# Performance work log

Measured on AMD Instinct MI355X. Metric: run time of the kernel, lower is better.

The kernel has to match this reference:

```python
import jax, jax.numpy as jnp
import numpy as np

D_MODEL = 1152
NUM_HEADS = 16
HEAD_DIM = D_MODEL // NUM_HEADS
B, N, M = 8, 4096, 300


def setup_inputs() -> dict:
    key = jax.random.key(0)
    ks = jax.random.split(key, 10)
    s = 0.02
    x = jax.random.normal(ks[0], (B, N, D_MODEL), dtype=jnp.float32)
    cond = jax.random.normal(ks[1], (B, M, D_MODEL), dtype=jnp.float32)
    # per-sample valid conditioning lengths in [1, M]
    mask = jax.random.randint(ks[2], (B,), 1, M + 1, dtype=jnp.int32)
    wq = jax.random.normal(ks[3], (D_MODEL, D_MODEL), dtype=jnp.float32) * s
    bq = jnp.zeros((D_MODEL,), dtype=jnp.float32)
    wkv = jax.random.normal(ks[4], (D_MODEL, 2 * D_MODEL), dtype=jnp.float32) * s
    bkv = jnp.zeros((2 * D_MODEL,), dtype=jnp.float32)
    wp = jax.random.normal(ks[5], (D_MODEL, D_MODEL), dtype=jnp.float32) * s
    bp = jnp.zeros((D_MODEL,), dtype=jnp.float32)
    return {"x": x, "cond": cond, "mask": mask, "wq": wq, "bq": bq,
            "wkv": wkv, "bkv": bkv, "wp": wp, "bp": bp}


def reference(x, cond, mask, wq, bq, wkv, bkv, wp, bp):
    b, n, c = x.shape
    m = cond.shape[1]
    # projections
    q = (x @ wq + bq).reshape(b, n, NUM_HEADS, HEAD_DIM)
    kv = (cond @ wkv + bkv).reshape(b, m, 2, NUM_HEADS, HEAD_DIM)
    k, v = kv[:, :, 0], kv[:, :, 1]
    scale = 1.0 / jnp.sqrt(jnp.asarray(HEAD_DIM, dtype=x.dtype))
    # [b, h, n, m] attention scores
    scores = jnp.einsum("bnhd,bmhd->bhnm", q, k) * scale
    # key positions j < mask[i] are valid (matches torch bool attn_mask)
    valid = (jnp.arange(m)[None, :] < mask[:, None])  # [b, m]
    bias = jnp.where(valid, 0.0, -1e9).astype(scores.dtype)[:, None, None, :]
    attn = jax.nn.softmax(scores + bias, axis=-1)
    out = jnp.einsum("bhnm,bmhd->bnhd", attn, v).reshape(b, n, c)
    return out @ wp + bp
```

## Files before the change

kernel.cpp:

```cpp
#include <hip/hip_runtime.h>
#include <cstdint>

typedef unsigned short u16;
typedef __attribute__((ext_vector_type(8))) short short8;
typedef __attribute__((ext_vector_type(4))) float floatx4;

__device__ __forceinline__ u16 f2bf(float f) {
    unsigned u = __float_as_uint(f);
    u += 0x7FFFu + ((u >> 16) & 1u);
    return (u16)(u >> 16);
}

__device__ __forceinline__ void async16(const void* g, void* l) {
    __builtin_amdgcn_global_load_lds(
        (const __attribute__((address_space(1))) unsigned*)g,
        (__attribute__((address_space(3))) unsigned*)l, 16, 0, 0);
}

__global__ void cast_bf16_kernel(const float* __restrict__ in, u16* __restrict__ out, long n8) {
    long i = (long)blockIdx.x * 256 + threadIdx.x;
    if (i >= n8) return;
    const float4* p = (const float4*)in;
    float4 a = p[i * 2], b = p[i * 2 + 1];
    uint4 o;
    o.x = f2bf(a.x) | ((unsigned)f2bf(a.y) << 16);
    o.y = f2bf(a.z) | ((unsigned)f2bf(a.w) << 16);
    o.z = f2bf(b.x) | ((unsigned)f2bf(b.y) << 16);
    o.w = f2bf(b.z) | ((unsigned)f2bf(b.w) << 16);
    ((uint4*)out)[i] = o;
}

__global__ void fill_zero(uint4* __restrict__ p, int n) {
    int i = blockIdx.x * 256 + threadIdx.x;
    if (i < n) p[i] = (uint4){0u, 0u, 0u, 0u};
}

__global__ void transpose_cast(const float* __restrict__ W, u16* __restrict__ Wt, int K, int N) {
    __shared__ float tile[32][33];
    int bx = blockIdx.x * 32, by = blockIdx.y * 32;
    int tx = threadIdx.x, ty = threadIdx.y;
#pragma unroll
    for (int i = 0; i < 32; i += 8)
        tile[ty + i][tx] = W[(long)(by + ty + i) * N + bx + tx];
    __syncthreads();
#pragma unroll
    for (int i = 0; i < 32; i += 8)
        Wt[(long)(bx + ty + i) * K + by + tx] = f2bf(tile[tx][ty + i]);
}

template <int MODE>
__global__ __launch_bounds__(256)
void gemm_bt(const u16* __restrict__ A, const u16* __restrict__ Bt,
             const float* __restrict__ bias, float scale,
             u16* __restrict__ outA, u16* __restrict__ outB, float* __restrict__ outF,
             int M, int N, int K) {
    __shared__ u16 As[128 * 32];
    __shared__ u16 Bs[128 * 32];
    const int tid = threadIdx.x, lane = tid & 63, wave = tid >> 6;
    const int wm = wave >> 1, wn = wave & 1;
    const int quad = lane >> 4, cl = lane & 15;
    const long rowBase = (long)blockIdx.x * 128;
    const int colBase = blockIdx.y * 128;
    const int srow = lane >> 2;
    const int skc = (lane & 3) * 8;

    floatx4 acc[4][4];
#pragma unroll
    for (int i = 0; i < 4; i++)
#pragma unroll
        for (int j = 0; j < 4; j++) acc[i][j] = (floatx4){0.f, 0.f, 0.f, 0.f};

    for (int k0 = 0; k0 < K; k0 += 32) {
#pragma unroll
        for (int j = 0; j < 2; ++j) {
            int inst = wave * 2 + j;
            long r = rowBase + inst * 16 + srow;
            if (r > (long)M - 1) r = (long)M - 1;
            async16(A + r * K + k0 + skc, &As[inst * 512]);
        }
#pragma unroll
        for (int j = 0; j < 2; ++j) {
            int inst = wave * 2 + j;
            long r = colBase + inst * 16 + srow;
            async16(Bt + r * K + k0 + skc, &Bs[inst * 512]);
        }
        __syncthreads();
        short8 af[4], bf[4];
#pragma unroll
        for (int mi = 0; mi < 4; mi++)
            af[mi] = *(const short8*)&As[(wm * 64 + mi * 16 + cl) * 32 + quad * 8];
#pragma unroll
        for (int ni = 0; ni < 4; ni++)
            bf[ni] = *(const short8*)&Bs[(wn * 64 + ni * 16 + cl) * 32 + quad * 8];
#pragma unroll
        for (int mi = 0; mi < 4; mi++)
#pragma unroll
            for (int ni = 0; ni < 4; ni++)
                acc[mi][ni] = __builtin_amdgcn_mfma_f32_16x16x32_bf16(af[mi], bf[ni], acc[mi][ni], 0, 0, 0);
        __syncthreads();
    }

#pragma unroll
    for (int mi = 0; mi < 4; mi++) {
        long row0 = rowBase + wm * 64 + mi * 16 + quad * 4;
#pragma unroll
        for (int ni = 0; ni < 4; ni++) {
            int col = colBase + wn * 64 + ni * 16 + cl;
            float bv = bias[col];
#pragma unroll
            for (int r = 0; r < 4; r++) {
                long row = row0 + r;
                if (row < M) {
                    float v = (acc[mi][ni][r] + bv) * scale;
                    if (MODE == 0) {
                        outA[row * N + col] = f2bf(v);
                    } else if (MODE == 1) {
                        int bb = (int)(row / 300);
                        int mm = (int)(row - (long)bb * 300);
                        if (col < 1152) {
                            int hh = col / 72, dd = col - hh * 72;
                            outA[((long)(bb * 16 + hh) * 384 + mm) * 72 + dd] = f2bf(v);
                        } else {
                            int c2 = col - 1152;
                            int hh = c2 / 72, dd = c2 - hh * 72;
                            int ch = mm >> 7, mc = mm & 127;
                            int g = (mc >> 3) ^ (dd & 7);
                            outB[(((long)(bb * 16 + hh) * 3 + ch) * 72 + dd) * 128 + g * 8 + (mc & 7)] = f2bf(v);
                        }
                    } else {
                        outF[row * (long)N + col] = v;
                    }
                }
            }
        }
    }
}

__global__ __launch_bounds__(256, 4)
void attn_kernel(const u16* __restrict__ Q, const u16* __restrict__ K,
                 const u16* __restrict__ V, const int* __restrict__ mask,
                 u16* __restrict__ O) {
    __shared__ __align__(16) u16 smem[(18432 + 20480) / 2];
    u16* Ks = smem;
    u16* Vs = smem + 9216;

    const int tid = threadIdx.x, lane = tid & 63, wave = tid >> 6;
    const int quad = lane >> 4, cl = lane & 15;
    const int b = blockIdx.z, h = blockIdx.y, nt = blockIdx.x;
    int mb = mask[b];
    if (mb > 300) mb = 300;
    if (mb < 1) mb = 1;
    const int bh = b * 16 + h;

    const long qbase = ((long)b * 4096 + nt * 64) * 1152 + h * 72;

    const u16* qrow = Q + qbase + (long)(wave * 16 + cl) * 1152;
    short8 zero8 = {0, 0, 0, 0, 0, 0, 0, 0};
    short8 aq[3];
    aq[0] = *(const short8*)(qrow + quad * 8);
    aq[1] = *(const short8*)(qrow + 32 + quad * 8);
    aq[2] = (quad == 0) ? *(const short8*)(qrow + 64) : zero8;

    if (tid < 16) {
        unsigned fill = 0x3F803F80u;
        *(uint4*)&Vs[72 * 128 + tid * 8] = (uint4){fill, fill, fill, fill};
    }

    floatx4 oacc[5];
#pragma unroll
    for (int i = 0; i < 5; i++) oacc[i] = (floatx4){0.f, 0.f, 0.f, 0.f};

    const u16* kb = K + (long)bh * 384 * 72;
    const u16* vb = V + (long)bh * 3 * 9216;

    const int nch = (mb + 127) >> 7;
    for (int ch = 0; ch < nch; ++ch) {
        const int base = ch << 7;
        __syncthreads();

        const u16* ksrc = kb + (long)base * 72;
        for (int i = wave; i < 18; i += 4)
            async16(ksrc + i * 512 + lane * 8, Ks + i * 512);
        const u16* vsrc = vb + (long)ch * 9216;
        for (int i = wave; i < 18; i += 4)
            async16(vsrc + i * 512 + lane * 8, Vs + i * 512);
        __syncthreads();

        floatx4 sacc[8];
#pragma unroll
        for (int t = 0; t < 8; t++) sacc[t] = (floatx4){0.f, 0.f, 0.f, 0.f};
#pragma unroll
        for (int kk = 0; kk < 3; ++kk) {
#pragma unroll
            for (int t = 0; t < 8; ++t) {
                short8 bfr = *(const short8*)&Ks[(t * 16 + cl) * 72 + kk * 32 + quad * 8];
                sacc[t] = __builtin_amdgcn_mfma_f32_16x16x32_bf16(aq[kk], bfr, sacc[t], 0, 0, 0);
            }
        }
        __syncthreads();

#pragma unroll
        for (int r = 0; r < 4; ++r) {
            int prow = (wave * 16 + quad * 4 + r) * 136;
#pragma unroll
            for (int t = 0; t < 8; ++t) {
                int col = base + t * 16 + cl;
                float p = (col < mb) ? __expf(sacc[t][r]) : 0.f;
                unsigned pb = f2bf(p);
                unsigned ob = __shfl_xor(pb, 1);
                if (!(lane & 1))
                    *(unsigned*)&Ks[prow + t * 16 + cl] = pb | (ob << 16);
            }
        }

#pragma unroll
        for (int kk = 0; kk < 4; ++kk) {
            short8 pf = *(const short8*)&Ks[(wave * 16 + cl) * 136 + kk * 32 + quad * 8];
#pragma unroll
            for (int dt = 0; dt < 5; ++dt) {
                int dd = dt * 16 + cl;
                short8 vf = *(const short8*)&Vs[dd * 128 + (((kk * 4 + quad) ^ (dd & 7)) << 3)];
                oacc[dt] = __builtin_amdgcn_mfma_f32_16x16x32_bf16(pf, vf, oacc[dt], 0, 0, 0);
            }
        }
    }

#pragma unroll
    for (int r = 0; r < 4; r++) {
        float l = __shfl(oacc[4][r], (lane & 48) + 8);
        float inv = 1.0f / l;
        int row = wave * 16 + quad * 4 + r;
#pragma unroll
        for (int dt = 0; dt < 5; dt++) {
            int dd = dt * 16 + cl;
            if (dd < 72) O[qbase + (long)row * 1152 + dd] = f2bf(oacc[dt][r] * inv);
        }
    }
}

extern "C" void kernel_launch(void* const* d_in, const int* in_sizes, int n_in,
                              void* d_out, int out_size, void* d_ws, size_t ws_size,
                              hipStream_t stream) {
    const float* x    = (const float*)d_in[0];
    const float* cond = (const float*)d_in[1];
    const int*   mask = (const int*)d_in[2];
    const float* wq   = (const float*)d_in[3];
    const float* bq   = (const float*)d_in[4];
    const float* wkv  = (const float*)d_in[5];
    const float* bkv  = (const float*)d_in[6];
    const float* wp   = (const float*)d_in[7];
    const float* bp   = (const float*)d_in[8];

    char* ws = (char*)d_ws;
    u16* xb    = (u16*)(ws);
    u16* condb = (u16*)(ws + 75497472ll);
    u16* wkvT  = (u16*)(ws + 81027072ll);
    u16* qbuf  = (u16*)(ws + 86335488ll);
    u16* kbuf  = (u16*)(ws + 161832960ll);
    u16* vbuf  = (u16*)(ws + 168910848ll);
    u16* wqT   = (u16*)(ws + 161832960ll);
    u16* wpT   = (u16*)(ws + 161832960ll);
    if (ws_size < 175988736ull) return;

    cast_bf16_kernel<<<18432, 256, 0, stream>>>(x, xb, 4718592ll);
    cast_bf16_kernel<<<1350, 256, 0, stream>>>(cond, condb, 345600ll);
    transpose_cast<<<dim3(36, 36), dim3(32, 8), 0, stream>>>(wq, wqT, 1152, 1152);
    transpose_cast<<<dim3(72, 36), dim3(32, 8), 0, stream>>>(wkv, wkvT, 1152, 2304);

    gemm_bt<0><<<dim3(256, 9), 256, 0, stream>>>(xb, wqT, bq, 0.11785113019775793f,
                                                 qbuf, nullptr, nullptr, 32768, 1152, 1152);
    fill_zero<<<3456, 256, 0, stream>>>((uint4*)kbuf, 884736);
    gemm_bt<1><<<dim3(19, 18), 256, 0, stream>>>(condb, wkvT, bkv, 1.0f,
                                                 kbuf, vbuf, nullptr, 2400, 2304, 1152);
    attn_kernel<<<dim3(64, 16, 8), 256, 0, stream>>>(qbuf, kbuf, vbuf, mask, xb);
    transpose_cast<<<dim3(36, 36), dim3(32, 8), 0, stream>>>(wp, wpT, 1152, 1152);
    gemm_bt<2><<<dim3(256, 9), 256, 0, stream>>>(xb, wpT, bp, 1.0f,
                                                 nullptr, nullptr, (float*)d_out, 32768, 1152, 1152);
}
```

Before: 689.8 us.

## Replace Q and output projection GEMMs with 256x256 double-buffered async-LDS kernel

Adds a 512-thread GEMM with 256x256 tiles, 64-wide K steps, double-buffered global_load_lds staging into swizzled LDS, and a four-phase MFMA schedule that interleaves prefetch with compute using s_setprio and partial vmcnt waits. Block ids are remapped in groups of eight to improve L2 reuse. Because 1152 columns is not a multiple of 256, the weight buffers are zero-padded to 1280 rows and output stores are masked. The aim is higher MFMA utilisation and less global traffic for the two large projections, at the cost of 128KB of dynamic LDS, heavy register use, and intricate wait counts that must be exactly right.

```diff
diff --git a/kernel.cpp b/kernel.cpp
--- a/kernel.cpp
+++ b/kernel.cpp
@@ -46,6 +46,157 @@
 #pragma unroll
     for (int i = 0; i < 32; i += 8)
         Wt[(long)(bx + ty + i) * K + by + tx] = f2bf(tile[tx][ty + i]);
+}
+
+template <int MODE>
+__global__ __launch_bounds__(512, 2)
+void gemm8p(const u16* __restrict__ A, const u16* __restrict__ Bt,
+            const float* __restrict__ bias, float scale,
+            u16* __restrict__ outA, float* __restrict__ outF) {
+    extern __shared__ u16 smem[];
+    const int K = 1152;
+    const int tid = threadIdx.x, lane = tid & 63, wave = tid >> 6;
+    const int quad = lane >> 4, cl = lane & 15;
+    const int wm = wave >> 2, wn = wave & 3;
+    const int l3 = lane >> 3, l7 = lane & 7;
+
+    int bid = blockIdx.x;
+    int swz = (bid & 7) * 80 + (bid >> 3);
+    int colTile = swz % 5, rowTile = swz / 5;
+    const long rowBase = (long)rowTile * 256;
+    const int colBase = colTile * 256;
+
+    const int sg = (l7 ^ l3) * 8;
+    const u16* pA = A + (rowBase + (wave >> 2) * 128 + (wave & 3) * 16 + l3) * (long)K + sg;
+    const u16* pB = Bt + ((long)colBase + (wave >> 1) * 64 + (wave & 1) * 16 + l3) * (long)K + sg;
+    const int dA0 = ((wave >> 2) * 128 + (wave & 3) * 16) * 64;
+    const int dB0 = ((wave >> 1) * 64 + (wave & 1) * 16) * 64;
+
+    auto stA = [&](int Ts, int h) {
+        const u16* s = pA + (long)(h * 64) * K + Ts * 64;
+        int d = (Ts & 1) * 16384 + dA0 + h * 4096;
+        async16(s, &smem[d]);
+        async16(s + 8 * K, &smem[d + 512]);
+    };
+    auto stB = [&](int Ts, int h) {
+        const u16* s = pB + (long)(h * 32) * K + Ts * 64;
+        int d = 32768 + (Ts & 1) * 16384 + dB0 + h * 2048;
+        async16(s, &smem[d]);
+        async16(s + 8 * K, &smem[d + 512]);
+    };
+
+    const int arow = wm * 8192 + cl * 64;
+    const int brow = wn * 4096 + cl * 64;
+    const int gs[2] = {((quad) ^ (cl & 7)) * 8, ((4 + quad) ^ (cl & 7)) * 8};
+
+    floatx4 acc[8][4];
+#pragma unroll
+    for (int i = 0; i < 8; i++)
+#pragma unroll
+        for (int j = 0; j < 4; j++) acc[i][j] = (floatx4){0.f, 0.f, 0.f, 0.f};
+
+#pragma unroll
+    for (int Ts = 0; Ts < 2; ++Ts) {
+        stA(Ts, 0); stB(Ts, 0); stA(Ts, 1); stB(Ts, 1);
+    }
+    asm volatile("s_waitcnt vmcnt(12)\n\ts_barrier" ::: "memory");
+
+#pragma unroll 2
+    for (int T = 0; T < 18; ++T) {
+        const int ab = (T & 1) * 16384;
+        const int bb = 32768 + (T & 1) * 16384;
+        const int t2 = T + 2;
+        const bool st = (t2 < 18);
+        short8 a0[2][4], a1[2][4], b0[2][2], b1[2][2];
+
+#pragma unroll
+        for (int kk = 0; kk < 2; ++kk) {
+#pragma unroll
+            for (int mi = 0; mi < 4; ++mi)
+                a0[kk][mi] = *(const short8*)&smem[ab + arow + mi * 1024 + gs[kk]];
+#pragma unroll
+            for (int ni = 0; ni < 2; ++ni)
+                b0[kk][ni] = *(const short8*)&smem[bb + brow + ni * 1024 + gs[kk]];
+        }
+        asm volatile("s_barrier" ::: "memory");
+        __builtin_amdgcn_s_setprio(1);
+#pragma unroll
+        for (int kk = 0; kk < 2; ++kk)
+#pragma unroll
+            for (int mi = 0; mi < 4; ++mi)
+#pragma unroll
+                for (int ni = 0; ni < 2; ++ni)
+                    acc[mi][ni] = __builtin_amdgcn_mfma_f32_16x16x32_bf16(a0[kk][mi], b0[kk][ni], acc[mi][ni], 0, 0, 0);
+        __builtin_amdgcn_s_setprio(0);
+        asm volatile("s_waitcnt vmcnt(10) lgkmcnt(0)\n\ts_barrier" ::: "memory");
+
+#pragma unroll
+        for (int kk = 0; kk < 2; ++kk)
+#pragma unroll
+            for (int mi = 0; mi < 4; ++mi)
+                a1[kk][mi] = *(const short8*)&smem[ab + arow + 4096 + mi * 1024 + gs[kk]];
+        if (st) { stA(t2, 0); stB(t2, 0); }
+        asm volatile("s_barrier" ::: "memory");
+        __builtin_amdgcn_s_setprio(1);
+#pragma unroll
+        for (int kk = 0; kk < 2; ++kk)
+#pragma unroll
+            for (int mi = 0; mi < 4; ++mi)
+#pragma unroll
+                for (int ni = 0; ni < 2; ++ni)
+                    acc[mi + 4][ni] = __builtin_amdgcn_mfma_f32_16x16x32_bf16(a1[kk][mi], b0[kk][ni], acc[mi + 4][ni], 0, 0, 0);
+        __builtin_amdgcn_s_setprio(0);
+        asm volatile("s_waitcnt vmcnt(12) lgkmcnt(0)\n\ts_barrier" ::: "memory");
+
+#pragma unroll
+        for (int kk = 0; kk < 2; ++kk)
+#pragma unroll
+            for (int ni = 0; ni < 2; ++ni)
+                b1[kk][ni] = *(const short8*)&smem[bb + brow + 2048 + ni * 1024 + gs[kk]];
+        if (st) stA(t2, 1);
+        asm volatile("s_barrier" ::: "memory");
+        __builtin_amdgcn_s_setprio(1);
+#pragma unroll
+        for (int kk = 0; kk < 2; ++kk)
+#pragma unroll
+            for (int mi = 0; mi < 4; ++mi)
+#pragma unroll
+                for (int ni = 0; ni < 2; ++ni)
+                    acc[mi][ni + 2] = __builtin_amdgcn_mfma_f32_16x16x32_bf16(a0[kk][mi], b1[kk][ni], acc[mi][ni + 2], 0, 0, 0);
+        __builtin_amdgcn_s_setprio(0);
+        asm volatile("s_waitcnt lgkmcnt(0)\n\ts_barrier" ::: "memory");
+
+        if (st) stB(t2, 1);
+        asm volatile("s_barrier" ::: "memory");
+        __builtin_amdgcn_s_setprio(1);
+#pragma unroll
+        for (int kk = 0; kk < 2; ++kk)
+#pragma unroll
+            for (int mi = 0; mi < 4; ++mi)
+#pragma unroll
+                for (int ni = 0; ni < 2; ++ni)
+                    acc[mi + 4][ni + 2] = __builtin_amdgcn_mfma_f32_16x16x32_bf16(a1[kk][mi], b1[kk][ni], acc[mi + 4][ni + 2], 0, 0, 0);
+        __builtin_amdgcn_s_setprio(0);
+        asm volatile("s_waitcnt vmcnt(10)\n\ts_barrier" ::: "memory");
+    }
+
+#pragma unroll
+    for (int mi = 0; mi < 8; ++mi) {
+        long row = rowBase + wm * 128 + mi * 16 + quad * 4;
+#pragma unroll
+        for (int ni = 0; ni < 4; ++ni) {
+            int col = colBase + wn * 64 + ni * 16 + cl;
+            if (col < 1152) {
+                float bv = bias[col];
+#pragma unroll
+                for (int r = 0; r < 4; ++r) {
+                    float v = (acc[mi][ni][r] + bv) * scale;
+                    if (MODE == 0) outA[(row + r) * 1152 + col] = f2bf(v);
+                    else           outF[(row + r) * 1152L + col] = v;
+                }
+            }
+        }
+    }
 }
 
 template <int MODE>
@@ -112,9 +263,7 @@
                 long row = row0 + r;
                 if (row < M) {
                     float v = (acc[mi][ni][r] + bv) * scale;
-                    if (MODE == 0) {
-                        outA[row * N + col] = f2bf(v);
-                    } else if (MODE == 1) {
+                    if (MODE == 1) {
                         int bb = (int)(row / 300);
                         int mm = (int)(row - (long)bb * 300);
                         if (col < 1152) {
@@ -127,8 +276,6 @@
                             int g = (mc >> 3) ^ (dd & 7);
                             outB[(((long)(bb * 16 + hh) * 3 + ch) * 72 + dd) * 128 + g * 8 + (mc & 7)] = f2bf(v);
                         }
-                    } else {
-                        outF[row * (long)N + col] = v;
                     }
                 }
             }
@@ -262,18 +409,28 @@
     u16* wpT   = (u16*)(ws + 161832960ll);
     if (ws_size < 175988736ull) return;
 
+    static bool s_attr = false;
+    if (!s_attr) {
+        hipFuncSetAttribute((const void*)gemm8p<0>, hipFuncAttributeMaxDynamicSharedMemorySize, 131072);
+        hipFuncSetAttribute((const void*)gemm8p<2>, hipFuncAttributeMaxDynamicSharedMemorySize, 131072);
+        s_attr = true;
+    }
+
     cast_bf16_kernel<<<18432, 256, 0, stream>>>(x, xb, 4718592ll);
     cast_bf16_kernel<<<1350, 256, 0, stream>>>(cond, condb, 345600ll);
+
+    fill_zero<<<72, 256, 0, stream>>>((uint4*)((char*)wqT + 2654208ll), 18432);
     transpose_cast<<<dim3(36, 36), dim3(32, 8), 0, stream>>>(wq, wqT, 1152, 1152);
     transpose_cast<<<dim3(72, 36), dim3(32, 8), 0, stream>>>(wkv, wkvT, 1152, 2304);
 
-    gemm_bt<0><<<dim3(256, 9), 256, 0, stream>>>(xb, wqT, bq, 0.11785113019775793f,
-                                                 qbuf, nullptr, nullptr, 32768, 1152, 1152);
+    gemm8p<0><<<640, 512, 131072, stream>>>(xb, wqT, bq, 0.11785113019775793f, qbuf, nullptr);
+
     fill_zero<<<3456, 256, 0, stream>>>((uint4*)kbuf, 884736);
     gemm_bt<1><<<dim3(19, 18), 256, 0, stream>>>(condb, wkvT, bkv, 1.0f,
                                                  kbuf, vbuf, nullptr, 2400, 2304, 1152);
     attn_kernel<<<dim3(64, 16, 8), 256, 0, stream>>>(qbuf, kbuf, vbuf, mask, xb);
+
+    fill_zero<<<72, 256, 0, stream>>>((uint4*)((char*)wpT + 2654208ll), 18432);
     transpose_cast<<<dim3(36, 36), dim3(32, 8), 0, stream>>>(wp, wpT, 1152, 1152);
-    gemm_bt<2><<<dim3(256, 9), 256, 0, stream>>>(xb, wpT, bp, 1.0f,
-                                                 nullptr, nullptr, (float*)d_out, 32768, 1152, 1152);
-}
+    gemm8p<2><<<640, 512, 131072, stream>>>(xb, wpT, bp, 1.0f, nullptr, (float*)d_out);
+}
```

Result: faster. 653.8 us (-5.2%).

## Replace Q and output projection GEMMs with 8-wave pipelined 256x192 tile kernel

Applied to the files above, without the earlier changes.

Adds a new GEMM kernel with 512 threads, 256x192 output tiles and double-buffered LDS holding K=64 slabs in 112KB of dynamic shared memory. Loads go straight to LDS asynchronously, with XOR-swizzled layout, and are prefetched two stages ahead. Explicit waitcnt, barriers and s_setprio let MFMA work overlap the loads, and a swizzled block order is meant to improve L2 reuse. The aim is to replace the simple single-buffered 128x128 GEMM on the two large 32768x1152x1152 projections and cut load stalls. The cost is hand-written synchronisation that is brittle and hardcoded to K=1152 and these shapes.

```diff
diff --git a/kernel.cpp b/kernel.cpp
--- a/kernel.cpp
+++ b/kernel.cpp
@@ -4,6 +4,9 @@
 typedef unsigned short u16;
 typedef __attribute__((ext_vector_type(8))) short short8;
 typedef __attribute__((ext_vector_type(4))) float floatx4;
+
+#define BAR()      __builtin_amdgcn_s_barrier()
+#define SCHEDBAR() __builtin_amdgcn_sched_barrier(0)
 
 __device__ __forceinline__ u16 f2bf(float f) {
     unsigned u = __float_as_uint(f);
@@ -46,6 +49,171 @@
 #pragma unroll
     for (int i = 0; i < 32; i += 8)
         Wt[(long)(bx + ty + i) * K + by + tx] = f2bf(tile[tx][ty + i]);
+}
+
+__device__ __forceinline__ void rd8(short8 (&a)[2][4], const u16* sm, int base, int g0, int g1) {
+#pragma unroll
+    for (int mi = 0; mi < 4; ++mi) {
+        a[0][mi] = *(const short8*)&sm[base + mi * 1024 + g0];
+        a[1][mi] = *(const short8*)&sm[base + mi * 1024 + g1];
+    }
+}
+__device__ __forceinline__ void rd6(short8 (&b)[2][3], const u16* sm, int base, int g0, int g1) {
+#pragma unroll
+    for (int ni = 0; ni < 3; ++ni) {
+        b[0][ni] = *(const short8*)&sm[base + ni * 1024 + g0];
+        b[1][ni] = *(const short8*)&sm[base + ni * 1024 + g1];
+    }
+}
+__device__ __forceinline__ void mfma24(floatx4 (&ah)[4][3], const short8 (&a)[2][4], const short8 (&b)[2][3]) {
+#pragma unroll
+    for (int kk = 0; kk < 2; ++kk)
+#pragma unroll
+        for (int mi = 0; mi < 4; ++mi)
+#pragma unroll
+            for (int ni = 0; ni < 3; ++ni)
+                ah[mi][ni] = __builtin_amdgcn_mfma_f32_16x16x32_bf16(a[kk][mi], b[kk][ni], ah[mi][ni], 0, 0, 0);
+}
+
+template <int MODE>
+__global__ __launch_bounds__(512, 2)
+void gemm8p(const u16* __restrict__ A, const u16* __restrict__ Bt,
+            const float* __restrict__ bias, float scale,
+            u16* __restrict__ outA, float* __restrict__ outF) {
+    extern __shared__ u16 smem[];
+    const int K = 1152;
+    const int tid = threadIdx.x, lane = tid & 63, wave = tid >> 6;
+    const int quad = lane >> 4, cl = lane & 15;
+    const int wm = wave >> 2, wn = wave & 3;
+    const int l3 = lane >> 3, l7 = lane & 7;
+    const int w8 = wave * 8;
+
+    int bid = blockIdx.x;
+    int swz = (bid & 7) * 96 + (bid >> 3);
+    int colTile = swz % 6, rowTile = swz / 6;
+    const long rowBase = (long)rowTile * 256;
+    const int colBase = colTile * 192;
+
+    const int sg = (l7 ^ l3) * 8;
+    const u16* pA = A + (rowBase + l3) * (long)K + sg;
+    const u16* pB = Bt + ((long)colBase + l3) * (long)K + sg;
+
+    auto stA = [&](int Ts, int r0) {
+        async16(pA + (long)r0 * K + Ts * 64, &smem[(Ts & 1) * 16384 + r0 * 64]);
+    };
+    auto stB = [&](int Ts, int r0) {
+        async16(pB + (long)r0 * K + Ts * 64, &smem[32768 + (Ts & 1) * 12288 + r0 * 64]);
+    };
+
+    const int arow = wm * 8192 + cl * 64;
+    const int brow = wn * 3072 + cl * 64;
+    const int gs0 = (quad ^ (cl & 7)) * 8;
+    const int gs1 = ((4 + quad) ^ (cl & 7)) * 8;
+
+    floatx4 acc[2][4][3];
+#pragma unroll
+    for (int h = 0; h < 2; ++h)
+#pragma unroll
+        for (int i = 0; i < 4; ++i)
+#pragma unroll
+            for (int j = 0; j < 3; ++j) acc[h][i][j] = (floatx4){0.f, 0.f, 0.f, 0.f};
+
+    short8 a0[2][4], a1[2][4], bf[2][3];
+
+    stA(0, w8); stA(0, 128 + w8);
+    stB(0, w8); stB(0, 64 + w8); stB(0, 128 + w8);
+    stA(0, 64 + w8); stA(0, 192 + w8);
+    stA(1, w8); stA(1, 128 + w8);
+    stB(1, w8); stB(1, 64 + w8); stB(1, 128 + w8);
+    SCHEDBAR();
+    asm volatile("s_waitcnt vmcnt(7)");
+    SCHEDBAR();
+    BAR();
+
+#pragma unroll 2
+    for (int T = 0; T < 16; ++T) {
+        const int ab = (T & 1) * 16384;
+        const int bb = 32768 + (T & 1) * 12288;
+        rd8(a0, smem, ab + arow, gs0, gs1);
+        rd6(bf, smem, bb + brow, gs0, gs1);
+        stA(T + 1, 64 + w8); stA(T + 1, 192 + w8);
+        SCHEDBAR(); BAR();
+        asm volatile("s_waitcnt lgkmcnt(0)"); SCHEDBAR();
+        __builtin_amdgcn_s_setprio(1);
+        mfma24(acc[0], a0, bf);
+        __builtin_amdgcn_s_setprio(0);
+        SCHEDBAR();
+        asm volatile("s_waitcnt vmcnt(7)"); SCHEDBAR(); BAR();
+        rd8(a1, smem, ab + arow + 4096, gs0, gs1);
+        stA(T + 2, w8); stA(T + 2, 128 + w8);
+        stB(T + 2, w8); stB(T + 2, 64 + w8); stB(T + 2, 128 + w8);
+        SCHEDBAR(); BAR();
+        asm volatile("s_waitcnt lgkmcnt(0)"); SCHEDBAR();
+        __builtin_amdgcn_s_setprio(1);
+        mfma24(acc[1], a1, bf);
+        __builtin_amdgcn_s_setprio(0);
+        SCHEDBAR();
+        asm volatile("s_waitcnt vmcnt(7)"); SCHEDBAR(); BAR();
+    }
+
+    {
+        const int ab = 0, bb = 32768;
+        rd8(a0, smem, ab + arow, gs0, gs1);
+        rd6(bf, smem, bb + brow, gs0, gs1);
+        stA(17, 64 + w8); stA(17, 192 + w8);
+        SCHEDBAR(); BAR();
+        asm volatile("s_waitcnt lgkmcnt(0)"); SCHEDBAR();
+        __builtin_amdgcn_s_setprio(1);
+        mfma24(acc[0], a0, bf);
+        __builtin_amdgcn_s_setprio(0);
+        SCHEDBAR();
+        asm volatile("s_waitcnt vmcnt(7)"); SCHEDBAR(); BAR();
+        rd8(a1, smem, ab + arow + 4096, gs0, gs1);
+        SCHEDBAR(); BAR();
+        asm volatile("s_waitcnt lgkmcnt(0)"); SCHEDBAR();
+        __builtin_amdgcn_s_setprio(1);
+        mfma24(acc[1], a1, bf);
+        __builtin_amdgcn_s_setprio(0);
+        SCHEDBAR();
+        asm volatile("s_waitcnt vmcnt(2)"); SCHEDBAR(); BAR();
+    }
+    {
+        const int ab = 16384, bb = 32768 + 12288;
+        rd8(a0, smem, ab + arow, gs0, gs1);
+        rd6(bf, smem, bb + brow, gs0, gs1);
+        SCHEDBAR(); BAR();
+        asm volatile("s_waitcnt lgkmcnt(0)"); SCHEDBAR();
+        __builtin_amdgcn_s_setprio(1);
+        mfma24(acc[0], a0, bf);
+        __builtin_amdgcn_s_setprio(0);
+        SCHEDBAR();
+        asm volatile("s_waitcnt vmcnt(0)"); SCHEDBAR(); BAR();
+        rd8(a1, smem, ab + arow + 4096, gs0, gs1);
+        SCHEDBAR();
+        asm volatile("s_waitcnt lgkmcnt(0)"); SCHEDBAR();
+        __builtin_amdgcn_s_setprio(1);
+        mfma24(acc[1], a1, bf);
+        __builtin_amdgcn_s_setprio(0);
+        SCHEDBAR();
+    }
+
+#pragma unroll
+    for (int h = 0; h < 2; ++h)
+#pragma unroll
+        for (int mi = 0; mi < 4; ++mi) {
+            long row = rowBase + wm * 128 + (h * 4 + mi) * 16 + quad * 4;
+#pragma unroll
+            for (int ni = 0; ni < 3; ++ni) {
+                int col = colBase + wn * 48 + ni * 16 + cl;
+                float bv = bias[col];
+#pragma unroll
+                for (int r = 0; r < 4; ++r) {
+                    float v = (acc[h][mi][ni][r] + bv) * scale;
+                    if (MODE == 0) outA[(row + r) * 1152 + col] = f2bf(v);
+                    else           outF[(row + r) * 1152L + col] = v;
+                }
+            }
+        }
 }
 
 template <int MODE>
@@ -85,18 +253,18 @@
             async16(Bt + r * K + k0 + skc, &Bs[inst * 512]);
         }
         __syncthreads();
-        short8 af[4], bf[4];
+        short8 af[4], bfr[4];
 #pragma unroll
         for (int mi = 0; mi < 4; mi++)
             af[mi] = *(const short8*)&As[(wm * 64 + mi * 16 + cl) * 32 + quad * 8];
 #pragma unroll
         for (int ni = 0; ni < 4; ni++)
-            bf[ni] = *(const short8*)&Bs[(wn * 64 + ni * 16 + cl) * 32 + quad * 8];
+            bfr[ni] = *(const short8*)&Bs[(wn * 64 + ni * 16 + cl) * 32 + quad * 8];
 #pragma unroll
         for (int mi = 0; mi < 4; mi++)
 #pragma unroll
             for (int ni = 0; ni < 4; ni++)
-                acc[mi][ni] = __builtin_amdgcn_mfma_f32_16x16x32_bf16(af[mi], bf[ni], acc[mi][ni], 0, 0, 0);
+                acc[mi][ni] = __builtin_amdgcn_mfma_f32_16x16x32_bf16(af[mi], bfr[ni], acc[mi][ni], 0, 0, 0);
         __syncthreads();
     }
 
@@ -112,9 +280,7 @@
                 long row = row0 + r;
                 if (row < M) {
                     float v = (acc[mi][ni][r] + bv) * scale;
-                    if (MODE == 0) {
-                        outA[row * N + col] = f2bf(v);
-                    } else if (MODE == 1) {
+                    if (MODE == 1) {
                         int bb = (int)(row / 300);
                         int mm = (int)(row - (long)bb * 300);
                         if (col < 1152) {
@@ -127,8 +293,6 @@
                             int g = (mc >> 3) ^ (dd & 7);
                             outB[(((long)(bb * 16 + hh) * 3 + ch) * 72 + dd) * 128 + g * 8 + (mc & 7)] = f2bf(v);
                         }
-                    } else {
-                        outF[row * (long)N + col] = v;
                     }
                 }
             }
@@ -262,18 +426,26 @@
     u16* wpT   = (u16*)(ws + 161832960ll);
     if (ws_size < 175988736ull) return;
 
+    static bool s_attr = false;
+    if (!s_attr) {
+        hipFuncSetAttribute((const void*)gemm8p<0>, hipFuncAttributeMaxDynamicSharedMemorySize, 114688);
+        hipFuncSetAttribute((const void*)gemm8p<2>, hipFuncAttributeMaxDynamicSharedMemorySize, 114688);
+        s_attr = true;
+    }
+
     cast_bf16_kernel<<<18432, 256, 0, stream>>>(x, xb, 4718592ll);
     cast_bf16_kernel<<<1350, 256, 0, stream>>>(cond, condb, 345600ll);
+
     transpose_cast<<<dim3(36, 36), dim3(32, 8), 0, stream>>>(wq, wqT, 1152, 1152);
     transpose_cast<<<dim3(72, 36), dim3(32, 8), 0, stream>>>(wkv, wkvT, 1152, 2304);
 
-    gemm_bt<0><<<dim3(256, 9), 256, 0, stream>>>(xb, wqT, bq, 0.11785113019775793f,
-                                                 qbuf, nullptr, nullptr, 32768, 1152, 1152);
+    gemm8p<0><<<768, 512, 114688, stream>>>(xb, wqT, bq, 0.11785113019775793f, qbuf, nullptr);
+
     fill_zero<<<3456, 256, 0, stream>>>((uint4*)kbuf, 884736);
     gemm_bt<1><<<dim3(19, 18), 256, 0, stream>>>(condb, wkvT, bkv, 1.0f,
                                                  kbuf, vbuf, nullptr, 2400, 2304, 1152);
     attn_kernel<<<dim3(64, 16, 8), 256, 0, stream>>>(qbuf, kbuf, vbuf, mask, xb);
+
     transpose_cast<<<dim3(36, 36), dim3(32, 8), 0, stream>>>(wp, wpT, 1152, 1152);
-    gemm_bt<2><<<dim3(256, 9), 256, 0, stream>>>(xb, wpT, bp, 1.0f,
-                                                 nullptr, nullptr, (float*)d_out, 32768, 1152, 1152);
-}
+    gemm8p<2><<<768, 512, 114688, stream>>>(xb, wpT, bp, 1.0f, nullptr, (float*)d_out);
+}
```

Result: faster. 616.8 us (-10.6%).
